# Performance work log

Hardware: AMD Instinct MI355X
Metric: run time of the kernel (lower is better)

## Reference

```python
import jax, jax.numpy as jnp
import numpy as np

S, B, H = 2048, 2, 1024
NH = 16
HD = H // NH  # 64


def setup_inputs() -> dict:
    key = jax.random.key(0)
    k1, k2 = jax.random.split(key)
    hidden_states = jax.random.normal(k1, (S, B, H), dtype=jnp.float32)
    W_qkv = jax.random.normal(k2, (3 * H, H), dtype=jnp.float32) * (H ** -0.5)
    b_qkv = jnp.zeros((3 * H,), dtype=jnp.float32)
    return {"hidden_states": hidden_states, "W_qkv": W_qkv, "b_qkv": b_qkv}


def reference(hidden_states, W_qkv, b_qkv):
    s, b, h = hidden_states.shape
    # QKV projection: [S,B,3H] -> [S,B,NH,3*HD] -> split
    qkv = hidden_states @ W_qkv.T + b_qkv
    qkv = qkv.reshape(s, b, NH, 3 * HD)
    q, k, v = jnp.split(qkv, 3, axis=-1)  # each [S,B,NH,HD]
    norm_factor = HD ** -0.5
    # scores: [B,NH,Sq,Sk]
    scores = jnp.einsum('sbhd,tbhd->bhst', q, k) * norm_factor
    # Cumsum sequence-op (seq_op_in_fp32=True): cumsum over key dim, scaled by Sq^-0.5
    probs = jnp.cumsum(scores.astype(jnp.float32), axis=-1) * (s ** -0.5)
    probs = probs.astype(hidden_states.dtype)
    # PV: [B,NH,Sq,HD] -> seq-first [Sq,B,NH*HD]
    ctx = jnp.einsum('bhst,tbhd->sbhd', probs, v)
    return ctx.reshape(s, b, h)
```

## Files before the change

kernel.cpp:

```cpp
#include <hip/hip_runtime.h>

#define S 2048
#define B 2
#define H 1024
#define NH 16
#define HD 64
#define THREE_H 3072
#define ROWS (S*B)

typedef __attribute__((ext_vector_type(8))) short short8;
typedef __attribute__((ext_vector_type(4))) float f32x4;
typedef const __attribute__((address_space(1))) unsigned int* gptr_t;
typedef __attribute__((address_space(3))) unsigned int* lptr_t;

#define N8_A (ROWS * H / 8)
#define N8_W (THREE_H * H / 8)

__device__ __forceinline__ ushort f2bf(float f) {
    union { float f; unsigned u; } v; v.f = f;
    unsigned r = v.u + 0x7fffu + ((v.u >> 16) & 1u);
    return (ushort)(r >> 16);
}
__device__ __forceinline__ float bf2f(ushort u) {
    union { unsigned u; float f; } v; v.u = ((unsigned)u) << 16;
    return v.f;
}

__global__ void cast_both(const float* __restrict__ A, const float* __restrict__ W,
                          ushort* __restrict__ Ab, ushort* __restrict__ Wb) {
    int i = blockIdx.x * 256 + threadIdx.x;
    const float4* s4;
    ushort* dst;
    if (i < N8_A) { s4 = (const float4*)A; dst = Ab; }
    else if (i < N8_A + N8_W) { s4 = (const float4*)W; dst = Wb; i -= N8_A; }
    else return;
    float4 a = s4[2 * i], b = s4[2 * i + 1];
    short8 o;
    o[0] = f2bf(a.x); o[1] = f2bf(a.y); o[2] = f2bf(a.z); o[3] = f2bf(a.w);
    o[4] = f2bf(b.x); o[5] = f2bf(b.y); o[6] = f2bf(b.z); o[7] = f2bf(b.w);
    *(short8*)(dst + 8 * (size_t)i) = o;
}

__global__ __launch_bounds__(256) void qkv_gemm_mfma(const ushort* __restrict__ Abf,
                                                     const ushort* __restrict__ Wbf,
                                                     const float* __restrict__ bias,
                                                     ushort* __restrict__ Qb,
                                                     ushort* __restrict__ Ktd,
                                                     ushort* __restrict__ Vtd) {
    __shared__ ushort Abuf[128 * 32];
    __shared__ ushort Bbuf[128 * 32];
    const int tid = threadIdx.x;
    const int wave = tid >> 6, lane = tid & 63;
    const int wr = wave >> 1, wc = wave & 1;
    const int row0 = blockIdx.x * 128;
    const int col0 = blockIdx.y * 128;

    f32x4 acc[4][4] = {};

    const int lrow = lane >> 2;
    const int gk = ((lane & 3) ^ (lrow & 3)) * 8;
    const int il = lane & 15, ko = lane >> 4;

    for (int k0 = 0; k0 < H; k0 += 32) {
#pragma unroll
        for (int p = 0; p < 2; ++p) {
            int c = wave * 2 + p;
            int row = c * 16 + lrow;
            __builtin_amdgcn_global_load_lds(
                (gptr_t)&Abf[(size_t)(row0 + row) * H + k0 + gk],
                (lptr_t)&Abuf[c * 512 + lane * 8], 16, 0, 0);
            __builtin_amdgcn_global_load_lds(
                (gptr_t)&Wbf[(size_t)(col0 + row) * H + k0 + gk],
                (lptr_t)&Bbuf[c * 512 + lane * 8], 16, 0, 0);
        }
        __syncthreads();

        short8 af[4], bfr[4];
#pragma unroll
        for (int m = 0; m < 4; ++m) {
            int ar = wr * 64 + m * 16 + il;
            int br = wc * 64 + m * 16 + il;
            af[m]  = *(const short8*)&Abuf[ar * 32 + (ko ^ (ar & 3)) * 8];
            bfr[m] = *(const short8*)&Bbuf[br * 32 + (ko ^ (br & 3)) * 8];
        }
#pragma unroll
        for (int m = 0; m < 4; ++m)
#pragma unroll
            for (int n = 0; n < 4; ++n)
                acc[m][n] = __builtin_amdgcn_mfma_f32_16x16x32_bf16(af[m], bfr[n], acc[m][n], 0, 0, 0);
        __syncthreads();
    }

#pragma unroll
    for (int n = 0; n < 4; ++n) {
        int cbase = col0 + wc * 64 + n * 16;
        int h   = cbase / 192;
        int r3  = cbase % 192;
        int sel = r3 >> 6;
        int d   = (r3 & 63) + il;
        float bv = bias[cbase + il];
        if (sel == 0) {
#pragma unroll
            for (int m = 0; m < 4; ++m) {
                int rowb = row0 + wr * 64 + m * 16 + ko * 4;
#pragma unroll
                for (int j = 0; j < 4; ++j) {
                    int r = rowb + j;
                    int s = r >> 1, b = r & 1;
                    Qb[((size_t)((b * NH + h) * S + s)) * HD + d] = f2bf(acc[m][n][j] + bv);
                }
            }
        } else {
            ushort* dst = (sel == 1) ? Ktd : Vtd;
            const size_t ro0 = ((size_t)(h)      * HD + d) * S;
            const size_t ro1 = ((size_t)(NH + h) * HD + d) * S;
#pragma unroll
            for (int m = 0; m < 4; ++m) {
                int t0 = (row0 + wr * 64 + m * 16 + ko * 4) >> 1;
                uint lo = (uint)f2bf(acc[m][n][0] + bv) |
                          ((uint)f2bf(acc[m][n][2] + bv) << 16);
                uint hi = (uint)f2bf(acc[m][n][1] + bv) |
                          ((uint)f2bf(acc[m][n][3] + bv) << 16);
                *(uint*)&dst[ro0 + t0] = lo;
                *(uint*)&dst[ro1 + t0] = hi;
            }
        }
    }
}

__global__ __launch_bounds__(256) void vscan(ushort* __restrict__ Vtd) {
    const int row = blockIdx.x * 4 + (threadIdx.x >> 6);
    const int lane = threadIdx.x & 63;
    ushort* vp = Vtd + (size_t)row * S + lane * 32;
    float v[32];
#pragma unroll
    for (int q = 0; q < 4; ++q) {
        short8 x = *(const short8*)(vp + q * 8);
#pragma unroll
        for (int k = 0; k < 8; ++k) v[q * 8 + k] = bf2f((ushort)x[k]);
    }
    float sum = 0.f;
#pragma unroll
    for (int k = 0; k < 32; ++k) sum += v[k];
    float t = sum;
#pragma unroll
    for (int off = 1; off < 64; off <<= 1) {
        float o = __shfl_down(t, off, 64);
        if (lane + off < 64) t += o;
    }
    float acc = t - sum;
#pragma unroll
    for (int k = 31; k >= 0; --k) { acc += v[k]; v[k] = acc; }
#pragma unroll
    for (int q = 0; q < 4; ++q) {
        short8 o;
#pragma unroll
        for (int k = 0; k < 8; ++k) o[k] = f2bf(v[q * 8 + k]);
        *(short8*)(vp + q * 8) = o;
    }
}

__global__ __launch_bounds__(256) void kvm_mfma(const ushort* __restrict__ Kt,
                                                const ushort* __restrict__ Vt,
                                                float* __restrict__ Mpart) {
    __shared__ float red[2][4096];
    const int bh = blockIdx.x, kb = blockIdx.y;
    const int tid = threadIdx.x, wave = tid >> 6, lane = tid & 63;
    const int slice = kb * 4 + wave;
    const ushort* Kp = Kt + (size_t)bh * HD * S;
    const ushort* Vp = Vt + (size_t)bh * HD * S;
    f32x4 acc[4][4] = {};
    const int il = lane & 15, g = lane >> 4;
    const int tbase = slice * 128 + g * 8;
#pragma unroll
    for (int ks = 0; ks < 4; ++ks) {
        const int t = tbase + ks * 32;
        short8 af[4], bfv[4];
#pragma unroll
        for (int m = 0; m < 4; ++m) af[m]  = *(const short8*)&Kp[(size_t)(m * 16 + il) * S + t];
#pragma unroll
        for (int n = 0; n < 4; ++n) bfv[n] = *(const short8*)&Vp[(size_t)(n * 16 + il) * S + t];
#pragma unroll
        for (int m = 0; m < 4; ++m)
#pragma unroll
            for (int n = 0; n < 4; ++n)
                acc[m][n] = __builtin_amdgcn_mfma_f32_16x16x32_bf16(af[m], bfv[n], acc[m][n], 0, 0, 0);
    }
#define DUMP(dstbuf)                                                        \
    { float* _d = (dstbuf);                                                 \
      _Pragma("unroll") for (int m = 0; m < 4; ++m)                         \
      _Pragma("unroll") for (int n = 0; n < 4; ++n)                         \
      _Pragma("unroll") for (int j = 0; j < 4; ++j)                         \
          _d[(m * 16 + g * 4 + j) * 64 + n * 16 + il] = acc[m][n][j]; }
#define ADDIN(srcbuf)                                                       \
    { const float* _s = (srcbuf);                                           \
      _Pragma("unroll") for (int m = 0; m < 4; ++m)                         \
      _Pragma("unroll") for (int n = 0; n < 4; ++n)                         \
      _Pragma("unroll") for (int j = 0; j < 4; ++j)                         \
          acc[m][n][j] += _s[(m * 16 + g * 4 + j) * 64 + n * 16 + il]; }
    if (wave == 1) DUMP(red[0]);
    if (wave == 3) DUMP(red[1]);
    __syncthreads();
    if (wave == 0) ADDIN(red[0]);
    if (wave == 2) ADDIN(red[1]);
    __syncthreads();
    if (wave == 2) DUMP(red[0]);
    __syncthreads();
    if (wave == 0) {
        ADDIN(red[0]);
        float* Mp = Mpart + ((size_t)kb * 32 + bh) * 4096;
#pragma unroll
        for (int m = 0; m < 4; ++m)
#pragma unroll
            for (int n = 0; n < 4; ++n)
#pragma unroll
                for (int j = 0; j < 4; ++j)
                    Mp[(m * 16 + g * 4 + j) * 64 + n * 16 + il] = acc[m][n][j];
    }
#undef DUMP
#undef ADDIN
}

__global__ __launch_bounds__(256) void qm_mfma(const ushort* __restrict__ Qb,
                                               const float* __restrict__ Mpart,
                                               float* __restrict__ out) {
    __shared__ ushort Mt[64][72];
    const int bh = blockIdx.x, b = bh >> 4, h = bh & 15;
    const int tid = threadIdx.x;
    {
        const int i = tid >> 2, jq = (tid & 3) * 16;
        f32x4 s0 = {}, s1 = {}, s2 = {}, s3 = {};
#pragma unroll
        for (int sl = 0; sl < 4; ++sl) {
            const float* p = Mpart + ((size_t)sl * 32 + bh) * 4096 + i * 64 + jq;
            s0 += *(const f32x4*)(p);
            s1 += *(const f32x4*)(p + 4);
            s2 += *(const f32x4*)(p + 8);
            s3 += *(const f32x4*)(p + 12);
        }
#pragma unroll
        for (int k = 0; k < 4; ++k) {
            Mt[jq + 0  + k][i] = f2bf(s0[k]);
            Mt[jq + 4  + k][i] = f2bf(s1[k]);
            Mt[jq + 8  + k][i] = f2bf(s2[k]);
            Mt[jq + 12 + k][i] = f2bf(s3[k]);
        }
    }
    __syncthreads();
    const int wave = tid >> 6, lane = tid & 63;
    const int sl15 = lane & 15, koct = (lane >> 4) * 8;
    const int s0b = blockIdx.y * 256 + wave * 64;
    f32x4 acc[4][4] = {};
#pragma unroll
    for (int ks = 0; ks < 2; ++ks) {
        short8 af[4], bfv[4];
#pragma unroll
        for (int m = 0; m < 4; ++m) {
            int s = s0b + m * 16 + sl15;
            af[m] = *(const short8*)&Qb[((size_t)bh * S + s) * HD + ks * 32 + koct];
        }
#pragma unroll
        for (int n = 0; n < 4; ++n)
            bfv[n] = *(const short8*)&Mt[n * 16 + sl15][ks * 32 + koct];
#pragma unroll
        for (int m = 0; m < 4; ++m)
#pragma unroll
            for (int n = 0; n < 4; ++n)
                acc[m][n] = __builtin_amdgcn_mfma_f32_16x16x32_bf16(af[m], bfv[n], acc[m][n], 0, 0, 0);
    }
    const float scale = 0.125f * 0.02209708691207961f;
#pragma unroll
    for (int m = 0; m < 4; ++m)
#pragma unroll
        for (int n = 0; n < 4; ++n)
#pragma unroll
            for (int j = 0; j < 4; ++j) {
                int s = s0b + m * 16 + (lane >> 4) * 4 + j;
                int d = n * 16 + sl15;
                out[(size_t)(s * B + b) * H + h * 64 + d] = acc[m][n][j] * scale;
            }
}

extern "C" void kernel_launch(void* const* d_in, const int* in_sizes, int n_in,
                              void* d_out, int out_size, void* d_ws, size_t ws_size,
                              hipStream_t stream) {
    const float* hidden = (const float*)d_in[0];
    const float* W      = (const float*)d_in[1];
    const float* bias   = (const float*)d_in[2];
    float* out = (float*)d_out;

    ushort* Qb    = (ushort*)d_ws;
    ushort* Ktd   = Qb + 4194304;
    ushort* Vtd   = Ktd + 4194304;
    float*  Mpart = (float*)(Vtd + 4194304);
    ushort* Abf   = (ushort*)(Mpart + 524288);
    ushort* Wbf   = Abf + 4194304;

    cast_both<<<(N8_A + N8_W + 255) / 256, 256, 0, stream>>>(hidden, W, Abf, Wbf);
    qkv_gemm_mfma<<<dim3(ROWS / 128, THREE_H / 128), 256, 0, stream>>>(Abf, Wbf, bias, Qb, Ktd, Vtd);
    vscan<<<512, 256, 0, stream>>>(Vtd);
    kvm_mfma<<<dim3(32, 4), 256, 0, stream>>>(Ktd, Vtd, Mpart);
    qm_mfma<<<dim3(32, 8), 256, 0, stream>>>(Qb, Mpart, out);
}
```

Baseline: 71.42 us.

## Fuse V scan, K^T V reduction and Q·M into one tail kernel

Replaces the three tail kernels (vscan, kvm_mfma, qm_mfma) with a single kernel. Each block owns one (batch, head) and a 16-column slice of the head dimension: it scans its own V rows, computes the full K^T·cumV slice over all keys with an in-LDS tree reduction across 8 waves, then multiplies Q by that slice directly. This removes two launches and the Mpart global round trip. The cost is only 128 blocks of work and per-block reloading of K and Q across the four dq slices. Separately, it changes the GEMM LDS swizzle to XOR with (row>>1)&3, intended to cut bank conflicts.

```diff
diff --git a/kernel.cpp b/kernel.cpp
--- a/kernel.cpp
+++ b/kernel.cpp
@@ -58,7 +58,7 @@
     f32x4 acc[4][4] = {};
 
     const int lrow = lane >> 2;
-    const int gk = ((lane & 3) ^ (lrow & 3)) * 8;
+    const int gk = ((lane & 3) ^ ((lrow >> 1) & 3)) * 8;
     const int il = lane & 15, ko = lane >> 4;
 
     for (int k0 = 0; k0 < H; k0 += 32) {
@@ -80,8 +80,8 @@
         for (int m = 0; m < 4; ++m) {
             int ar = wr * 64 + m * 16 + il;
             int br = wc * 64 + m * 16 + il;
-            af[m]  = *(const short8*)&Abuf[ar * 32 + (ko ^ (ar & 3)) * 8];
-            bfr[m] = *(const short8*)&Bbuf[br * 32 + (ko ^ (br & 3)) * 8];
+            af[m]  = *(const short8*)&Abuf[ar * 32 + (ko ^ ((ar >> 1) & 3)) * 8];
+            bfr[m] = *(const short8*)&Bbuf[br * 32 + (ko ^ ((br >> 1) & 3)) * 8];
         }
 #pragma unroll
         for (int m = 0; m < 4; ++m)
@@ -128,157 +128,117 @@
     }
 }
 
-__global__ __launch_bounds__(256) void vscan(ushort* __restrict__ Vtd) {
-    const int row = blockIdx.x * 4 + (threadIdx.x >> 6);
-    const int lane = threadIdx.x & 63;
-    ushort* vp = Vtd + (size_t)row * S + lane * 32;
-    float v[32];
-#pragma unroll
-    for (int q = 0; q < 4; ++q) {
-        short8 x = *(const short8*)(vp + q * 8);
-#pragma unroll
-        for (int k = 0; k < 8; ++k) v[q * 8 + k] = bf2f((ushort)x[k]);
-    }
-    float sum = 0.f;
-#pragma unroll
-    for (int k = 0; k < 32; ++k) sum += v[k];
-    float t = sum;
-#pragma unroll
-    for (int off = 1; off < 64; off <<= 1) {
-        float o = __shfl_down(t, off, 64);
-        if (lane + off < 64) t += o;
-    }
-    float acc = t - sum;
-#pragma unroll
-    for (int k = 31; k >= 0; --k) { acc += v[k]; v[k] = acc; }
-#pragma unroll
-    for (int q = 0; q < 4; ++q) {
-        short8 o;
-#pragma unroll
-        for (int k = 0; k < 8; ++k) o[k] = f2bf(v[q * 8 + k]);
-        *(short8*)(vp + q * 8) = o;
-    }
-}
-
-__global__ __launch_bounds__(256) void kvm_mfma(const ushort* __restrict__ Kt,
-                                                const ushort* __restrict__ Vt,
-                                                float* __restrict__ Mpart) {
-    __shared__ float red[2][4096];
-    const int bh = blockIdx.x, kb = blockIdx.y;
+__global__ __launch_bounds__(512) void tail_fused(const ushort* __restrict__ Ktd,
+                                                  ushort* __restrict__ Vtd,
+                                                  const ushort* __restrict__ Qb,
+                                                  float* __restrict__ out) {
+    __shared__ float red[4][1024];
+    __shared__ ushort Mt[16][72];
+    const int bh = blockIdx.x, dq = blockIdx.y;
+    const int b = bh >> 4, h = bh & 15;
     const int tid = threadIdx.x, wave = tid >> 6, lane = tid & 63;
-    const int slice = kb * 4 + wave;
-    const ushort* Kp = Kt + (size_t)bh * HD * S;
-    const ushort* Vp = Vt + (size_t)bh * HD * S;
-    f32x4 acc[4][4] = {};
     const int il = lane & 15, g = lane >> 4;
-    const int tbase = slice * 128 + g * 8;
-#pragma unroll
-    for (int ks = 0; ks < 4; ++ks) {
-        const int t = tbase + ks * 32;
-        short8 af[4], bfv[4];
-#pragma unroll
-        for (int m = 0; m < 4; ++m) af[m]  = *(const short8*)&Kp[(size_t)(m * 16 + il) * S + t];
-#pragma unroll
-        for (int n = 0; n < 4; ++n) bfv[n] = *(const short8*)&Vp[(size_t)(n * 16 + il) * S + t];
+
+#pragma unroll
+    for (int rr = 0; rr < 2; ++rr) {
+        const int d = dq * 16 + wave * 2 + rr;
+        ushort* vp = Vtd + ((size_t)bh * HD + d) * S + lane * 32;
+        float v[32];
+#pragma unroll
+        for (int q = 0; q < 4; ++q) {
+            short8 x = *(const short8*)(vp + q * 8);
+#pragma unroll
+            for (int k = 0; k < 8; ++k) v[q * 8 + k] = bf2f((ushort)x[k]);
+        }
+        float sum = 0.f;
+#pragma unroll
+        for (int k = 0; k < 32; ++k) sum += v[k];
+        float t = sum;
+#pragma unroll
+        for (int off = 1; off < 64; off <<= 1) {
+            float o = __shfl_down(t, off, 64);
+            if (lane + off < 64) t += o;
+        }
+        float a = t - sum;
+#pragma unroll
+        for (int k = 31; k >= 0; --k) { a += v[k]; v[k] = a; }
+#pragma unroll
+        for (int q = 0; q < 4; ++q) {
+            short8 o;
+#pragma unroll
+            for (int k = 0; k < 8; ++k) o[k] = f2bf(v[q * 8 + k]);
+            *(short8*)(vp + q * 8) = o;
+        }
+    }
+    __threadfence();
+    __syncthreads();
+
+    const ushort* Kp = Ktd + (size_t)bh * HD * S;
+    const ushort* Vp = Vtd + ((size_t)bh * HD + dq * 16) * S;
+    f32x4 macc[4] = {};
+    {
+        const int tb = wave * 256 + g * 8;
+#pragma unroll
+        for (int ks = 0; ks < 8; ++ks) {
+            const int t = tb + ks * 32;
+            short8 bv = *(const short8*)&Vp[(size_t)il * S + t];
+#pragma unroll
+            for (int m = 0; m < 4; ++m) {
+                short8 af = *(const short8*)&Kp[(size_t)(m * 16 + il) * S + t];
+                macc[m] = __builtin_amdgcn_mfma_f32_16x16x32_bf16(af, bv, macc[m], 0, 0, 0);
+            }
+        }
+    }
+
+#define MDUMP(buf) { float* _d = (buf);                                     \
+    _Pragma("unroll") for (int m = 0; m < 4; ++m)                           \
+    _Pragma("unroll") for (int j = 0; j < 4; ++j)                           \
+        _d[(m * 16 + g * 4 + j) * 16 + il] = macc[m][j]; }
+#define MADD(buf) { const float* _s = (buf);                                \
+    _Pragma("unroll") for (int m = 0; m < 4; ++m)                           \
+    _Pragma("unroll") for (int j = 0; j < 4; ++j)                           \
+        macc[m][j] += _s[(m * 16 + g * 4 + j) * 16 + il]; }
+    if (wave >= 4) MDUMP(red[wave - 4]);
+    __syncthreads();
+    if (wave < 4) MADD(red[wave]);
+    __syncthreads();
+    if (wave == 2 || wave == 3) MDUMP(red[wave - 2]);
+    __syncthreads();
+    if (wave < 2) MADD(red[wave]);
+    __syncthreads();
+    if (wave == 1) MDUMP(red[0]);
+    __syncthreads();
+    if (wave == 0) {
+        MADD(red[0]);
 #pragma unroll
         for (int m = 0; m < 4; ++m)
 #pragma unroll
-            for (int n = 0; n < 4; ++n)
-                acc[m][n] = __builtin_amdgcn_mfma_f32_16x16x32_bf16(af[m], bfv[n], acc[m][n], 0, 0, 0);
-    }
-#define DUMP(dstbuf)                                                        \
-    { float* _d = (dstbuf);                                                 \
-      _Pragma("unroll") for (int m = 0; m < 4; ++m)                         \
-      _Pragma("unroll") for (int n = 0; n < 4; ++n)                         \
-      _Pragma("unroll") for (int j = 0; j < 4; ++j)                         \
-          _d[(m * 16 + g * 4 + j) * 64 + n * 16 + il] = acc[m][n][j]; }
-#define ADDIN(srcbuf)                                                       \
-    { const float* _s = (srcbuf);                                           \
-      _Pragma("unroll") for (int m = 0; m < 4; ++m)                         \
-      _Pragma("unroll") for (int n = 0; n < 4; ++n)                         \
-      _Pragma("unroll") for (int j = 0; j < 4; ++j)                         \
-          acc[m][n][j] += _s[(m * 16 + g * 4 + j) * 64 + n * 16 + il]; }
-    if (wave == 1) DUMP(red[0]);
-    if (wave == 3) DUMP(red[1]);
-    __syncthreads();
-    if (wave == 0) ADDIN(red[0]);
-    if (wave == 2) ADDIN(red[1]);
-    __syncthreads();
-    if (wave == 2) DUMP(red[0]);
-    __syncthreads();
-    if (wave == 0) {
-        ADDIN(red[0]);
-        float* Mp = Mpart + ((size_t)kb * 32 + bh) * 4096;
-#pragma unroll
-        for (int m = 0; m < 4; ++m)
-#pragma unroll
-            for (int n = 0; n < 4; ++n)
-#pragma unroll
-                for (int j = 0; j < 4; ++j)
-                    Mp[(m * 16 + g * 4 + j) * 64 + n * 16 + il] = acc[m][n][j];
-    }
-#undef DUMP
-#undef ADDIN
-}
-
-__global__ __launch_bounds__(256) void qm_mfma(const ushort* __restrict__ Qb,
-                                               const float* __restrict__ Mpart,
-                                               float* __restrict__ out) {
-    __shared__ ushort Mt[64][72];
-    const int bh = blockIdx.x, b = bh >> 4, h = bh & 15;
-    const int tid = threadIdx.x;
-    {
-        const int i = tid >> 2, jq = (tid & 3) * 16;
-        f32x4 s0 = {}, s1 = {}, s2 = {}, s3 = {};
-#pragma unroll
-        for (int sl = 0; sl < 4; ++sl) {
-            const float* p = Mpart + ((size_t)sl * 32 + bh) * 4096 + i * 64 + jq;
-            s0 += *(const f32x4*)(p);
-            s1 += *(const f32x4*)(p + 4);
-            s2 += *(const f32x4*)(p + 8);
-            s3 += *(const f32x4*)(p + 12);
-        }
-#pragma unroll
-        for (int k = 0; k < 4; ++k) {
-            Mt[jq + 0  + k][i] = f2bf(s0[k]);
-            Mt[jq + 4  + k][i] = f2bf(s1[k]);
-            Mt[jq + 8  + k][i] = f2bf(s2[k]);
-            Mt[jq + 12 + k][i] = f2bf(s3[k]);
-        }
-    }
-    __syncthreads();
-    const int wave = tid >> 6, lane = tid & 63;
-    const int sl15 = lane & 15, koct = (lane >> 4) * 8;
-    const int s0b = blockIdx.y * 256 + wave * 64;
-    f32x4 acc[4][4] = {};
+            for (int j = 0; j < 4; ++j)
+                Mt[il][m * 16 + g * 4 + j] = f2bf(macc[m][j]);
+    }
+    __syncthreads();
+#undef MDUMP
+#undef MADD
+
+    const int s0b = wave * 256;
+    f32x4 qacc[16] = {};
 #pragma unroll
     for (int ks = 0; ks < 2; ++ks) {
-        short8 af[4], bfv[4];
-#pragma unroll
-        for (int m = 0; m < 4; ++m) {
-            int s = s0b + m * 16 + sl15;
-            af[m] = *(const short8*)&Qb[((size_t)bh * S + s) * HD + ks * 32 + koct];
-        }
-#pragma unroll
-        for (int n = 0; n < 4; ++n)
-            bfv[n] = *(const short8*)&Mt[n * 16 + sl15][ks * 32 + koct];
-#pragma unroll
-        for (int m = 0; m < 4; ++m)
-#pragma unroll
-            for (int n = 0; n < 4; ++n)
-                acc[m][n] = __builtin_amdgcn_mfma_f32_16x16x32_bf16(af[m], bfv[n], acc[m][n], 0, 0, 0);
+        short8 bv = *(const short8*)&Mt[il][ks * 32 + g * 8];
+#pragma unroll
+        for (int m = 0; m < 16; ++m) {
+            short8 af = *(const short8*)&Qb[((size_t)bh * S + s0b + m * 16 + il) * HD + ks * 32 + g * 8];
+            qacc[m] = __builtin_amdgcn_mfma_f32_16x16x32_bf16(af, bv, qacc[m], 0, 0, 0);
+        }
     }
     const float scale = 0.125f * 0.02209708691207961f;
 #pragma unroll
-    for (int m = 0; m < 4; ++m)
-#pragma unroll
-        for (int n = 0; n < 4; ++n)
-#pragma unroll
-            for (int j = 0; j < 4; ++j) {
-                int s = s0b + m * 16 + (lane >> 4) * 4 + j;
-                int d = n * 16 + sl15;
-                out[(size_t)(s * B + b) * H + h * 64 + d] = acc[m][n][j] * scale;
-            }
+    for (int m = 0; m < 16; ++m)
+#pragma unroll
+        for (int j = 0; j < 4; ++j) {
+            int s = s0b + m * 16 + g * 4 + j;
+            out[(size_t)(s * B + b) * H + h * 64 + dq * 16 + il] = qacc[m][j] * scale;
+        }
 }
 
 extern "C" void kernel_launch(void* const* d_in, const int* in_sizes, int n_in,
@@ -292,13 +252,10 @@
     ushort* Qb    = (ushort*)d_ws;
     ushort* Ktd   = Qb + 4194304;
     ushort* Vtd   = Ktd + 4194304;
-    float*  Mpart = (float*)(Vtd + 4194304);
-    ushort* Abf   = (ushort*)(Mpart + 524288);
+    ushort* Abf   = Vtd + 4194304;
     ushort* Wbf   = Abf + 4194304;
 
     cast_both<<<(N8_A + N8_W + 255) / 256, 256, 0, stream>>>(hidden, W, Abf, Wbf);
     qkv_gemm_mfma<<<dim3(ROWS / 128, THREE_H / 128), 256, 0, stream>>>(Abf, Wbf, bias, Qb, Ktd, Vtd);
-    vscan<<<512, 256, 0, stream>>>(Vtd);
-    kvm_mfma<<<dim3(32, 4), 256, 0, stream>>>(Ktd, Vtd, Mpart);
-    qm_mfma<<<dim3(32, 8), 256, 0, stream>>>(Qb, Mpart, out);
-}
+    tail_fused<<<dim3(32, 4), 512, 0, stream>>>(Ktd, Vtd, Qb, out);
+}
```

Measured after the change: 110.1 us. 1.54x slower.

## Rewrite QKV GEMM with 256x192 tiles, double-buffered LDS and phased prefetch

Applied to the files above, without the earlier changes.

The QKV projection GEMM goes from 128x128 tiles with a single LDS buffer and K-step 32 to 256x192 tiles with 512 threads, K-step 64 and double-buffered LDS. Global-to-LDS loads for the next tile are issued in stages across the four MFMA phases, using explicit vmcnt waits, raw s_barrier and setprio, so memory traffic overlaps compute. The aim is to hide load latency and raise operand reuse per block. The cost is fewer blocks in the grid (16x16), one block per CU occupancy, and much larger LDS and register use per block.

```diff
diff --git a/kernel.cpp b/kernel.cpp
--- a/kernel.cpp
+++ b/kernel.cpp
@@ -41,59 +41,94 @@
     *(short8*)(dst + 8 * (size_t)i) = o;
 }
 
-__global__ __launch_bounds__(256) void qkv_gemm_mfma(const ushort* __restrict__ Abf,
-                                                     const ushort* __restrict__ Wbf,
-                                                     const float* __restrict__ bias,
-                                                     ushort* __restrict__ Qb,
-                                                     ushort* __restrict__ Ktd,
-                                                     ushort* __restrict__ Vtd) {
-    __shared__ ushort Abuf[128 * 32];
-    __shared__ ushort Bbuf[128 * 32];
+__global__ __launch_bounds__(512, 1) void qkv_gemm_mfma(const ushort* __restrict__ Abf,
+                                                        const ushort* __restrict__ Wbf,
+                                                        const float* __restrict__ bias,
+                                                        ushort* __restrict__ Qb,
+                                                        ushort* __restrict__ Ktd,
+                                                        ushort* __restrict__ Vtd) {
+    __shared__ ushort Abuf[2][256 * 64];
+    __shared__ ushort Bbuf[2][192 * 64];
     const int tid = threadIdx.x;
     const int wave = tid >> 6, lane = tid & 63;
-    const int wr = wave >> 1, wc = wave & 1;
-    const int row0 = blockIdx.x * 128;
-    const int col0 = blockIdx.y * 128;
-
-    f32x4 acc[4][4] = {};
-
-    const int lrow = lane >> 2;
-    const int gk = ((lane & 3) ^ (lrow & 3)) * 8;
+    const int wr = wave >> 2, wc = wave & 3;
+    const int row0 = blockIdx.x * 256;
+    const int col0 = blockIdx.y * 192;
+
+    f32x4 acc[8][3] = {};
+
+    const int srow = lane >> 3;
+    const int gk = ((lane & 7) ^ srow) * 8;
     const int il = lane & 15, ko = lane >> 4;
 
-    for (int k0 = 0; k0 < H; k0 += 32) {
-#pragma unroll
-        for (int p = 0; p < 2; ++p) {
-            int c = wave * 2 + p;
-            int row = c * 16 + lrow;
-            __builtin_amdgcn_global_load_lds(
-                (gptr_t)&Abf[(size_t)(row0 + row) * H + k0 + gk],
-                (lptr_t)&Abuf[c * 512 + lane * 8], 16, 0, 0);
-            __builtin_amdgcn_global_load_lds(
-                (gptr_t)&Wbf[(size_t)(col0 + row) * H + k0 + gk],
-                (lptr_t)&Bbuf[c * 512 + lane * 8], 16, 0, 0);
-        }
-        __syncthreads();
-
-        short8 af[4], bfr[4];
-#pragma unroll
-        for (int m = 0; m < 4; ++m) {
-            int ar = wr * 64 + m * 16 + il;
-            int br = wc * 64 + m * 16 + il;
-            af[m]  = *(const short8*)&Abuf[ar * 32 + (ko ^ (ar & 3)) * 8];
-            bfr[m] = *(const short8*)&Bbuf[br * 32 + (ko ^ (br & 3)) * 8];
-        }
-#pragma unroll
-        for (int m = 0; m < 4; ++m)
-#pragma unroll
-            for (int n = 0; n < 4; ++n)
-                acc[m][n] = __builtin_amdgcn_mfma_f32_16x16x32_bf16(af[m], bfr[n], acc[m][n], 0, 0, 0);
-        __syncthreads();
-    }
-
-#pragma unroll
-    for (int n = 0; n < 4; ++n) {
-        int cbase = col0 + wc * 64 + n * 16;
+    size_t aSrc[4], bSrc[3];
+    int dOff[4];
+#pragma unroll
+    for (int c = 0; c < 4; ++c) {
+        aSrc[c] = (size_t)(row0 + c * 64 + wave * 8 + srow) * H + gk;
+        dOff[c] = (c * 64 + wave * 8) * 64 + lane * 8;
+    }
+#pragma unroll
+    for (int c = 0; c < 3; ++c)
+        bSrc[c] = (size_t)(col0 + c * 64 + wave * 8 + srow) * H + gk;
+
+#define GLD(srcp, dstp) __builtin_amdgcn_global_load_lds((gptr_t)(srcp), (lptr_t)(dstp), 16, 0, 0)
+#define ST_A(BUF, T, C) GLD(&Abf[aSrc[C] + (size_t)(T) * 64], &Abuf[BUF][dOff[C]])
+#define ST_B(BUF, T, C) GLD(&Wbf[bSrc[C] + (size_t)(T) * 64], &Bbuf[BUF][dOff[C]])
+
+#define PHASE(BUF, MH, KH, READB, BREG, STAGE_STMT)                          \
+    {                                                                        \
+        STAGE_STMT;                                                          \
+        short8 af[4];                                                        \
+        _Pragma("unroll") for (int mf = 0; mf < 4; ++mf) {                   \
+            int ar = wr * 128 + (MH) * 64 + mf * 16 + il;                    \
+            af[mf] = *(const short8*)&Abuf[BUF][ar * 64 + (((KH) * 4 + ko) ^ (ar & 7)) * 8]; \
+        }                                                                    \
+        if (READB) {                                                         \
+            _Pragma("unroll") for (int nf = 0; nf < 3; ++nf) {               \
+                int br = wc * 48 + nf * 16 + il;                             \
+                BREG[nf] = *(const short8*)&Bbuf[BUF][br * 64 + (((KH) * 4 + ko) ^ (br & 7)) * 8]; \
+            }                                                                \
+        }                                                                    \
+        __builtin_amdgcn_s_setprio(1);                                       \
+        _Pragma("unroll") for (int mf = 0; mf < 4; ++mf)                     \
+            _Pragma("unroll") for (int nf = 0; nf < 3; ++nf)                 \
+                acc[(MH) * 4 + mf][nf] = __builtin_amdgcn_mfma_f32_16x16x32_bf16( \
+                    af[mf], BREG[nf], acc[(MH) * 4 + mf][nf], 0, 0, 0);      \
+        __builtin_amdgcn_s_setprio(0);                                       \
+        asm volatile("s_barrier" ::: "memory");                              \
+    }
+
+    ST_A(0, 0, 0); ST_A(0, 0, 2);
+    ST_A(0, 0, 1); ST_A(0, 0, 3);
+    ST_B(0, 0, 0); ST_B(0, 0, 1); ST_B(0, 0, 2);
+    ST_A(1, 1, 0); ST_A(1, 1, 2);
+
+    short8 bfr0[3], bfr1[3];
+    for (int p = 0; p < 8; ++p) {
+        const int T = 2 * p;
+        asm volatile("s_waitcnt vmcnt(2)" ::: "memory");
+        asm volatile("s_barrier" ::: "memory");
+        PHASE(0, 0, 0, true,  bfr0, { ST_A(1, T + 1, 1); ST_A(1, T + 1, 3); });
+        PHASE(0, 1, 0, false, bfr0, { ST_B(1, T + 1, 0); ST_B(1, T + 1, 1); ST_B(1, T + 1, 2); });
+        PHASE(0, 0, 1, true,  bfr1, {});
+        PHASE(0, 1, 1, false, bfr1, { if (p < 7) { ST_A(0, T + 2, 0); ST_A(0, T + 2, 2); } });
+        if (p < 7) { asm volatile("s_waitcnt vmcnt(2)" ::: "memory"); }
+        else       { asm volatile("s_waitcnt vmcnt(0)" ::: "memory"); }
+        asm volatile("s_barrier" ::: "memory");
+        PHASE(1, 0, 0, true,  bfr0, { if (p < 7) { ST_A(0, T + 2, 1); ST_A(0, T + 2, 3); } });
+        PHASE(1, 1, 0, false, bfr0, { if (p < 7) { ST_B(0, T + 2, 0); ST_B(0, T + 2, 1); ST_B(0, T + 2, 2); } });
+        PHASE(1, 0, 1, true,  bfr1, {});
+        PHASE(1, 1, 1, false, bfr1, { if (p < 7) { ST_A(1, T + 3, 0); ST_A(1, T + 3, 2); } });
+    }
+#undef PHASE
+#undef ST_A
+#undef ST_B
+#undef GLD
+
+#pragma unroll
+    for (int nf = 0; nf < 3; ++nf) {
+        int cbase = col0 + wc * 48 + nf * 16;
         int h   = cbase / 192;
         int r3  = cbase % 192;
         int sel = r3 >> 6;
@@ -101,13 +136,13 @@
         float bv = bias[cbase + il];
         if (sel == 0) {
 #pragma unroll
-            for (int m = 0; m < 4; ++m) {
-                int rowb = row0 + wr * 64 + m * 16 + ko * 4;
+            for (int mi = 0; mi < 8; ++mi) {
+                int rowb = row0 + wr * 128 + mi * 16 + ko * 4;
 #pragma unroll
                 for (int j = 0; j < 4; ++j) {
                     int r = rowb + j;
                     int s = r >> 1, b = r & 1;
-                    Qb[((size_t)((b * NH + h) * S + s)) * HD + d] = f2bf(acc[m][n][j] + bv);
+                    Qb[((size_t)((b * NH + h) * S + s)) * HD + d] = f2bf(acc[mi][nf][j] + bv);
                 }
             }
         } else {
@@ -115,12 +150,12 @@
             const size_t ro0 = ((size_t)(h)      * HD + d) * S;
             const size_t ro1 = ((size_t)(NH + h) * HD + d) * S;
 #pragma unroll
-            for (int m = 0; m < 4; ++m) {
-                int t0 = (row0 + wr * 64 + m * 16 + ko * 4) >> 1;
-                uint lo = (uint)f2bf(acc[m][n][0] + bv) |
-                          ((uint)f2bf(acc[m][n][2] + bv) << 16);
-                uint hi = (uint)f2bf(acc[m][n][1] + bv) |
-                          ((uint)f2bf(acc[m][n][3] + bv) << 16);
+            for (int mi = 0; mi < 8; ++mi) {
+                int t0 = (row0 + wr * 128 + mi * 16 + ko * 4) >> 1;
+                uint lo = (uint)f2bf(acc[mi][nf][0] + bv) |
+                          ((uint)f2bf(acc[mi][nf][2] + bv) << 16);
+                uint hi = (uint)f2bf(acc[mi][nf][1] + bv) |
+                          ((uint)f2bf(acc[mi][nf][3] + bv) << 16);
                 *(uint*)&dst[ro0 + t0] = lo;
                 *(uint*)&dst[ro1 + t0] = hi;
             }
@@ -297,7 +332,7 @@
     ushort* Wbf   = Abf + 4194304;
 
     cast_both<<<(N8_A + N8_W + 255) / 256, 256, 0, stream>>>(hidden, W, Abf, Wbf);
-    qkv_gemm_mfma<<<dim3(ROWS / 128, THREE_H / 128), 256, 0, stream>>>(Abf, Wbf, bias, Qb, Ktd, Vtd);
+    qkv_gemm_mfma<<<dim3(ROWS / 256, THREE_H / 192), 512, 0, stream>>>(Abf, Wbf, bias, Qb, Ktd, Vtd);
     vscan<<<512, 256, 0, stream>>>(Vtd);
     kvm_mfma<<<dim3(32, 4), 256, 0, stream>>>(Ktd, Vtd, Mpart);
     qm_mfma<<<dim3(32, 8), 256, 0, stream>>>(Qb, Mpart, out);
```

After: 73.58 us. 1.03x slower.
